# Optimization experiments

Measured on AMD Instinct MI355X. Metric: run time of the kernel, lower is better.

Reference implementation:

```python
import jax, jax.numpy as jnp
import numpy as np

N_NODES = 50000
E_EDGES = 1600000
D = 256


def setup_inputs() -> dict:
    key = jax.random.key(0)
    ks = jax.random.split(key, 10)
    inp = {
        "x": jax.random.normal(ks[0], (N_NODES, D), dtype=jnp.float32),
        "W0": jax.random.normal(ks[1], (D, D), dtype=jnp.float32) * (1.0 / np.sqrt(D)),
        "W1": jax.random.normal(ks[2], (D, D), dtype=jnp.float32) * (1.0 / np.sqrt(D)),
        "b": jnp.zeros((D,), dtype=jnp.float32),
        "src0": jax.random.randint(ks[3], (E_EDGES,), 0, N_NODES, dtype=jnp.int32),
        "dst0": jax.random.randint(ks[4], (E_EDGES,), 0, N_NODES, dtype=jnp.int32),
        "val0": jax.random.uniform(ks[5], (E_EDGES,), dtype=jnp.float32),
        "src1": jax.random.randint(ks[6], (E_EDGES,), 0, N_NODES, dtype=jnp.int32),
        "dst1": jax.random.randint(ks[7], (E_EDGES,), 0, N_NODES, dtype=jnp.int32),
        "val1": jax.random.uniform(ks[8], (E_EDGES,), dtype=jnp.float32),
    }
    return inp


def _spmm(src, dst, val, dense, num_segments):
    # sparse [N,N] (COO: A[dst, src] = val) @ dense [N,D] -> [N,D]
    # gather rows of dense at src, scale by edge value, scatter-add to dst
    return jax.ops.segment_sum(val[:, None] * dense[src], dst, num_segments=num_segments)


def reference(x, W0, W1, b, src0, dst0, val0, src1, dst1, val1):
    n = x.shape[0]
    # per-support dense GEMM then SpMM, summed over supports (2 supports)
    out = _spmm(src0, dst0, val0, x @ W0, n)
    out = out + _spmm(src1, dst1, val1, x @ W1, n)
    out = out + b  # bias
    return jax.nn.relu(out)  # act = F.relu
```

## Files before the change

### kernel.cpp

```cpp
#include <hip/hip_runtime.h>

#define D 256
#define CAP 64
#define CAP_S 60
#define OVFCAP 16384
#define BCAP 10240
#define CHUNK 8192

typedef __attribute__((ext_vector_type(8))) short short8;
typedef __attribute__((ext_vector_type(4))) float f32x4;

__device__ inline ushort f2bf(float f) {
  unsigned u = __float_as_uint(f);
  unsigned r = (u + 0x7FFF + ((u >> 16) & 1)) >> 16;
  return (ushort)r;
}
__device__ inline float bf_lo(unsigned u) { return __uint_as_float(u << 16); }
__device__ inline float bf_hi(unsigned u) { return __uint_as_float(u & 0xFFFF0000u); }

__global__ __launch_bounds__(256) void prep_kernel(const float* __restrict__ W0,
                                                   const float* __restrict__ W1,
                                                   ushort* __restrict__ Wt0,
                                                   ushort* __restrict__ Wt1,
                                                   int* __restrict__ gz, int ngz) {
  if (blockIdx.x < 128) {
    const int blk = blockIdx.x;
    const float* W = (blk >> 6) ? W1 : W0;
    ushort* Wt = (blk >> 6) ? Wt1 : Wt0;
    __shared__ float t[32][33];
    int tx = threadIdx.x & 31, ty = threadIdx.x >> 5;
    int k0 = (blk & 7) * 32, n0 = ((blk >> 3) & 7) * 32;
    for (int r = ty; r < 32; r += 8)
      t[r][tx] = W[(size_t)(k0 + r) * D + n0 + tx];
    __syncthreads();
    for (int r = ty; r < 32; r += 8)
      Wt[(size_t)(n0 + r) * D + k0 + tx] = f2bf(t[tx][r]);
  } else {
    int nb = gridDim.x - 128;
    for (int i = (blockIdx.x - 128) * 256 + threadIdx.x; i < ngz; i += nb * 256)
      gz[i] = 0;
  }
}

__device__ __forceinline__ void gemm_body(const float* __restrict__ A,
                                          const ushort* __restrict__ Bt,
                                          ushort* __restrict__ C, int M,
                                          int blk, int mtiles) {
  __shared__ ushort As[128 * 40];
  __shared__ ushort Bs[128 * 40];
  const int tid = threadIdx.x;
  const int bm = (blk % mtiles) * 128;
  const int bn = (blk / mtiles) * 128;
  const int wave = tid >> 6, lane = tid & 63;
  const int wm = wave & 1, wn = wave >> 1;
  const int lr = lane & 15;
  const int kg = lane >> 4;
  f32x4 acc[4][4];
#pragma unroll
  for (int m = 0; m < 4; ++m)
#pragma unroll
    for (int n = 0; n < 4; ++n) acc[m][n] = (f32x4){0.f, 0.f, 0.f, 0.f};

  for (int k0 = 0; k0 < D; k0 += 32) {
    __syncthreads();
#pragma unroll
    for (int c = 0; c < 4; ++c) {
      int linear = c * 256 + tid;
      int row = linear >> 3;
      int f4 = linear & 7;
      int gr = bm + row;
      float4 a = (gr < M) ? *(const float4*)(A + (size_t)gr * D + k0 + f4 * 4)
                          : make_float4(0.f, 0.f, 0.f, 0.f);
      ushort4 o;
      o.x = f2bf(a.x); o.y = f2bf(a.y); o.z = f2bf(a.z); o.w = f2bf(a.w);
      *(ushort4*)&As[row * 40 + f4 * 4] = o;
    }
#pragma unroll
    for (int c = 0; c < 2; ++c) {
      int linear = c * 256 + tid;
      int row = linear >> 2;
      int part = linear & 3;
      uint4 w4 = *(const uint4*)(Bt + (size_t)(bn + row) * D + k0 + part * 8);
      *(uint4*)&Bs[row * 40 + part * 8] = w4;
    }
    __syncthreads();
    short8 af[4], bfr[4];
#pragma unroll
    for (int m = 0; m < 4; ++m)
      af[m] = *(const short8*)&As[(wm * 64 + m * 16 + lr) * 40 + kg * 8];
#pragma unroll
    for (int n = 0; n < 4; ++n)
      bfr[n] = *(const short8*)&Bs[(wn * 64 + n * 16 + lr) * 40 + kg * 8];
#pragma unroll
    for (int m = 0; m < 4; ++m)
#pragma unroll
      for (int n = 0; n < 4; ++n)
        acc[m][n] = __builtin_amdgcn_mfma_f32_16x16x32_bf16(af[m], bfr[n], acc[m][n], 0, 0, 0);
  }

#pragma unroll
  for (int m = 0; m < 4; ++m)
#pragma unroll
    for (int j = 0; j < 4; ++j) {
      int gr = bm + wm * 64 + m * 16 + kg * 4 + j;
      if (gr < M) {
#pragma unroll
        for (int n = 0; n < 4; ++n) {
          int gc = bn + wn * 64 + n * 16 + lr;
          C[(size_t)gr * D + gc] = f2bf(acc[m][n][j]);
        }
      }
    }
}

__device__ __forceinline__ void binA_body(const int* __restrict__ src,
                                          const int* __restrict__ dst,
                                          const float* __restrict__ val, int E,
                                          int* __restrict__ gcur,
                                          int2* __restrict__ binned,
                                          int* __restrict__ ovfc, int4* __restrict__ ovf,
                                          int nbkt, int blk) {
  __shared__ int hist[200];
  __shared__ int base[200];
  const int tid = threadIdx.x;
  for (int i = tid; i < nbkt; i += 256) hist[i] = 0;
  __syncthreads();
  const int e0 = blk * CHUNK;
  const int e1 = min(E, e0 + CHUNK);
  for (int e = e0 + tid; e < e1; e += 256)
    atomicAdd(&hist[dst[e] >> 8], 1);
  __syncthreads();
  for (int i = tid; i < nbkt; i += 256) {
    int h = hist[i];
    base[i] = h ? atomicAdd(&gcur[i], h) : 0;
    hist[i] = 0;
  }
  __syncthreads();
  for (int e = e0 + tid; e < e1; e += 256) {
    int d = dst[e];
    int s = src[e];
    int vb = __float_as_int(val[e]);
    int k = d >> 8;
    int pos = base[k] + atomicAdd(&hist[k], 1);
    if (pos < BCAP) {
      binned[(size_t)k * BCAP + pos] = make_int2(((d & 255) << 16) | s, vb);
    } else {
      int o = atomicAdd(ovfc, 1);
      if (o < OVFCAP) ovf[o] = make_int4(d, s, vb, 0);
    }
  }
}

__global__ __launch_bounds__(256) void passB(const int2* __restrict__ binned,
                                             const int* __restrict__ gcur,
                                             uint* __restrict__ padded,
                                             int* __restrict__ cnt,
                                             int* __restrict__ ovfc, int4* __restrict__ ovf) {
  __shared__ int lcnt[256];
  __shared__ uint stage[256 * CAP_S];
  const int b = blockIdx.x;
  const int tid = threadIdx.x;
  lcnt[tid] = 0;
  __syncthreads();
  const int n = min(gcur[b], BCAP);
  const int2* bp = binned + (size_t)b * BCAP;
  for (int i = tid; i < n; i += 256) {
    int2 e = bp[i];
    int dlow = (e.x >> 16) & 255;
    int s = atomicAdd(&lcnt[dlow], 1);
    if (s < CAP_S) {
      float v = __int_as_float(e.y);
      stage[dlow * CAP_S + s] = (uint)(e.x & 0xFFFF) | ((uint)f2bf(v) << 16);
    } else {
      int o = atomicAdd(ovfc, 1);
      if (o < OVFCAP) ovf[o] = make_int4((b << 8) + dlow, e.x & 0xFFFF, e.y, 0);
    }
  }
  __syncthreads();
  const int row = (b << 8) + tid;
  const int written = min(lcnt[tid], CAP_S);
  cnt[row] = written;
  uint4* dp = (uint4*)(padded + ((size_t)row << 6));
  const uint4* sp = (const uint4*)&stage[tid * CAP_S];
  const int nq = (written + 3) >> 2;
  for (int q = 0; q < nq; ++q) dp[q] = sp[q];
}

template <int FINAL>
__device__ __forceinline__ void spmm_body(const ushort* __restrict__ H,
                                          const uint* __restrict__ padded,
                                          const int* __restrict__ cnt,
                                          float* __restrict__ out,
                                          const float* __restrict__ bias, int N,
                                          int blk) {
  const int row = blk * 4 + (threadIdx.x >> 6);
  if (row >= N) return;
  const int lane = threadIdx.x & 63;
  const int c = min(cnt[row], CAP);
  const uint4* ep4 = (const uint4*)(padded + ((size_t)row << 6));
  float4 acc = make_float4(0.f, 0.f, 0.f, 0.f);
  const int nchunk = (c + 3) >> 2;
  if (nchunk > 0) {
    uint4 cur = ep4[0];
    for (int j = 0; j < nchunk; ++j) {
      uint4 nxt = (j + 1 < nchunk) ? ep4[j + 1] : cur;
      int b4 = j << 2;
#pragma unroll
      for (int k = 0; k < 4; ++k) {
        uint e = (k == 0) ? cur.x : (k == 1) ? cur.y : (k == 2) ? cur.z : cur.w;
        bool ok = (b4 + k) < c;
        uint sidx = ok ? (e & 0xFFFFu) : 0u;
        float v = ok ? __uint_as_float(e & 0xFFFF0000u) : 0.f;
        uint2 h = *((const uint2*)(H + (size_t)sidx * D) + lane);
        acc.x += v * bf_lo(h.x);
        acc.y += v * bf_hi(h.x);
        acc.z += v * bf_lo(h.y);
        acc.w += v * bf_hi(h.y);
      }
      cur = nxt;
    }
  }
  float4* op = (float4*)(out + (size_t)row * D) + lane;
  if (FINAL) {
    float4 o = *op;
    float4 bb = ((const float4*)bias)[lane];
    o.x = fmaxf(o.x + acc.x + bb.x, 0.f);
    o.y = fmaxf(o.y + acc.y + bb.y, 0.f);
    o.z = fmaxf(o.z + acc.z + bb.z, 0.f);
    o.w = fmaxf(o.w + acc.w + bb.w, 0.f);
    *op = o;
  } else {
    *op = acc;
  }
}

__global__ __launch_bounds__(256) void fatA(
    const float* __restrict__ A, const ushort* __restrict__ Bt0, ushort* __restrict__ H,
    int M, int mtiles,
    const int* __restrict__ src0, const int* __restrict__ dst0, const float* __restrict__ val0,
    int E0, int* __restrict__ gcur0, int2* __restrict__ binned0, int* __restrict__ ovfc0,
    int4* __restrict__ ovf0,
    const int* __restrict__ src1, const int* __restrict__ dst1, const float* __restrict__ val1,
    int E1, int* __restrict__ gcur1, int2* __restrict__ binned1, int* __restrict__ ovfc1,
    int4* __restrict__ ovf1,
    int nbkt, int nbA0, int nbA1) {
  const int bid = blockIdx.x;
  if (bid < nbA0)
    binA_body(src0, dst0, val0, E0, gcur0, binned0, ovfc0, ovf0, nbkt, bid);
  else if (bid < nbA0 + nbA1)
    binA_body(src1, dst1, val1, E1, gcur1, binned1, ovfc1, ovf1, nbkt, bid - nbA0);
  else
    gemm_body(A, Bt0, H, M, bid - nbA0 - nbA1, mtiles);
}

__global__ __launch_bounds__(256) void gemm_plain(const float* __restrict__ A,
                                                  const ushort* __restrict__ Bt,
                                                  ushort* __restrict__ C, int M, int mtiles) {
  gemm_body(A, Bt, C, M, blockIdx.x, mtiles);
}

__global__ __launch_bounds__(256) void spmm_first(const ushort* __restrict__ H,
                                                  const uint* __restrict__ padded,
                                                  const int* __restrict__ cnt,
                                                  float* __restrict__ out,
                                                  const float* __restrict__ bias, int N) {
  spmm_body<0>(H, padded, cnt, out, bias, N, blockIdx.x);
}

__global__ __launch_bounds__(256) void spmm_final(const ushort* __restrict__ H,
                                                  const uint* __restrict__ padded,
                                                  const int* __restrict__ cnt,
                                                  float* __restrict__ out,
                                                  const float* __restrict__ bias, int N) {
  spmm_body<1>(H, padded, cnt, out, bias, N, blockIdx.x);
}

__global__ void overflow_add(const int* __restrict__ ovfc, const int4* __restrict__ ovf,
                             const ushort* __restrict__ H, float* __restrict__ out) {
  int n = min(*ovfc, OVFCAP);
  int w = (blockIdx.x * blockDim.x + threadIdx.x) >> 6;
  int lane = threadIdx.x & 63;
  int nw = (gridDim.x * blockDim.x) >> 6;
  for (int i = w; i < n; i += nw) {
    int4 r = ovf[i];
    uint2 h = *((const uint2*)(H + (size_t)r.y * D) + lane);
    float v = __int_as_float(r.z);
    float* op = out + (size_t)r.x * D + (lane << 2);
    unsafeAtomicAdd(op + 0, v * bf_lo(h.x));
    unsafeAtomicAdd(op + 1, v * bf_hi(h.x));
    unsafeAtomicAdd(op + 2, v * bf_lo(h.y));
    unsafeAtomicAdd(op + 3, v * bf_hi(h.y));
  }
}

extern "C" void kernel_launch(void* const* d_in, const int* in_sizes, int n_in,
                              void* d_out, int out_size, void* d_ws, size_t ws_size,
                              hipStream_t stream) {
  const float* x    = (const float*)d_in[0];
  const float* W0   = (const float*)d_in[1];
  const float* W1   = (const float*)d_in[2];
  const float* b    = (const float*)d_in[3];
  const int*   src0 = (const int*)d_in[4];
  const int*   dst0 = (const int*)d_in[5];
  const float* val0 = (const float*)d_in[6];
  const int*   src1 = (const int*)d_in[7];
  const int*   dst1 = (const int*)d_in[8];
  const float* val1 = (const float*)d_in[9];
  float* out = (float*)d_out;

  const int N  = in_sizes[0] / D;
  const int E0 = in_sizes[4];
  const int E1 = in_sizes[7];
  const int nbkt = (N + 255) >> 8;
  const int nrows = nbkt << 8;

  char* w = (char*)d_ws;
  auto align = [](size_t v) { return (v + 255) & ~(size_t)255; };
  ushort* H       = (ushort*)w; w += align((size_t)N * D * 2);
  ushort* Wt0     = (ushort*)w; w += align((size_t)D * D * 2);
  ushort* Wt1     = (ushort*)w; w += align((size_t)D * D * 2);
  int2*   binned0 = (int2*)w;   w += align((size_t)nbkt * BCAP * 8);
  int2*   binned1 = (int2*)w;   w += align((size_t)nbkt * BCAP * 8);
  uint*   padded0 = (uint*)w;   w += align((size_t)nrows * CAP * 4);
  uint*   padded1 = (uint*)binned0;
  int*    cnt0    = (int*)w;    w += align((size_t)nrows * 4);
  int*    cnt1    = (int*)w;    w += align((size_t)nrows * 4);
  int*    gz      = (int*)w;    w += align((size_t)(2 * nbkt + 2) * 4);
  int4*   ovf0    = (int4*)w;   w += align((size_t)OVFCAP * 16);
  int4*   ovf1    = (int4*)w;   w += align((size_t)OVFCAP * 16);
  int* gcur0 = gz;
  int* gcur1 = gz + nbkt;
  int* ovfc0 = gz + 2 * nbkt;
  int* ovfc1 = gz + 2 * nbkt + 1;

  const int mtiles = (N + 127) / 128;
  const int NGB = mtiles * 2;
  const int nbA0 = (E0 + CHUNK - 1) / CHUNK;
  const int nbA1 = (E1 + CHUNK - 1) / CHUNK;
  const int NPB = (N + 3) / 4;

  prep_kernel<<<130, 256, 0, stream>>>(W0, W1, Wt0, Wt1, gz, 2 * nbkt + 2);
  fatA<<<nbA0 + nbA1 + NGB, 256, 0, stream>>>(
      x, Wt0, H, N, mtiles,
      src0, dst0, val0, E0, gcur0, binned0, ovfc0, ovf0,
      src1, dst1, val1, E1, gcur1, binned1, ovfc1, ovf1,
      nbkt, nbA0, nbA1);
  passB<<<nbkt, 256, 0, stream>>>(binned0, gcur0, padded0, cnt0, ovfc0, ovf0);
  spmm_first<<<NPB, 256, 0, stream>>>(H, padded0, cnt0, out, b, N);
  overflow_add<<<16, 256, 0, stream>>>(ovfc0, ovf0, H, out);
  gemm_plain<<<NGB, 256, 0, stream>>>(x, Wt1, H, N, mtiles);
  passB<<<nbkt, 256, 0, stream>>>(binned1, gcur1, padded1, cnt1, ovfc1, ovf1);
  overflow_add<<<16, 256, 0, stream>>>(ovfc1, ovf1, H, out);
  spmm_final<<<NPB, 256, 0, stream>>>(H, padded1, cnt1, out, b, N);
}
```

Measured before the change: 344.1 us.

## Fuse both supports' GEMMs, binning passes and SpMMs into single launches

When the workspace is large enough, both support GEMMs now run in one combined launch with separate H buffers, both passB binnings run in one grid, and a single fused SpMM kernel gathers both supports per row and applies bias and ReLU. Overflow rows are zeroed and flagged beforehand so the fused kernel can add the atomically accumulated overflow contributions. The gather loop is also rewritten to double-buffer index and H-row loads, so gathers are issued ahead of the multiply-adds. This drops the intermediate write and re-read of the output and gives each launch more parallelism, at the cost of extra workspace and a fallback path if the workspace is too small.

```diff
diff --git a/kernel.cpp b/kernel.cpp
--- a/kernel.cpp
+++ b/kernel.cpp
@@ -151,14 +151,14 @@
   }
 }
 
-__global__ __launch_bounds__(256) void passB(const int2* __restrict__ binned,
-                                             const int* __restrict__ gcur,
-                                             uint* __restrict__ padded,
-                                             int* __restrict__ cnt,
-                                             int* __restrict__ ovfc, int4* __restrict__ ovf) {
+__device__ __forceinline__ void passB_body(const int2* __restrict__ binned,
+                                           const int* __restrict__ gcur,
+                                           uint* __restrict__ padded,
+                                           int* __restrict__ cnt,
+                                           int* __restrict__ ovfc, int4* __restrict__ ovf,
+                                           int b) {
   __shared__ int lcnt[256];
   __shared__ uint stage[256 * CAP_S];
-  const int b = blockIdx.x;
   const int tid = threadIdx.x;
   lcnt[tid] = 0;
   __syncthreads();
@@ -180,10 +180,75 @@
   const int row = (b << 8) + tid;
   const int written = min(lcnt[tid], CAP_S);
   cnt[row] = written;
+  const int nq = (written + 3) >> 2;
+  for (int s = written; s < (nq << 2); ++s) stage[tid * CAP_S + s] = 0;
   uint4* dp = (uint4*)(padded + ((size_t)row << 6));
   const uint4* sp = (const uint4*)&stage[tid * CAP_S];
-  const int nq = (written + 3) >> 2;
   for (int q = 0; q < nq; ++q) dp[q] = sp[q];
+}
+
+__global__ __launch_bounds__(256) void passB(const int2* __restrict__ binned,
+                                             const int* __restrict__ gcur,
+                                             uint* __restrict__ padded,
+                                             int* __restrict__ cnt,
+                                             int* __restrict__ ovfc, int4* __restrict__ ovf) {
+  passB_body(binned, gcur, padded, cnt, ovfc, ovf, blockIdx.x);
+}
+
+__global__ __launch_bounds__(256) void passBoth(
+    const int2* __restrict__ binned0, const int* __restrict__ gcur0, uint* __restrict__ padded0,
+    int* __restrict__ cnt0, int* __restrict__ ovfc0, int4* __restrict__ ovf0,
+    const int2* __restrict__ binned1, const int* __restrict__ gcur1, uint* __restrict__ padded1,
+    int* __restrict__ cnt1, int* __restrict__ ovfc1, int4* __restrict__ ovf1, int nbkt) {
+  if (blockIdx.x < nbkt)
+    passB_body(binned0, gcur0, padded0, cnt0, ovfc0, ovf0, blockIdx.x);
+  else
+    passB_body(binned1, gcur1, padded1, cnt1, ovfc1, ovf1, blockIdx.x - nbkt);
+}
+
+__device__ __forceinline__ void gather_acc(const ushort* __restrict__ H,
+                                           const uint* __restrict__ padded,
+                                           int row, int c, int lane, float4& acc) {
+  const int nc = (c + 3) >> 2;
+  if (nc <= 0) return;
+  const uint4* ep4 = (const uint4*)(padded + ((size_t)row << 6));
+  const uint2* Hl = (const uint2*)H + lane;
+
+  uint2 h0[4], h1[4];
+  float v0[4], v1[4];
+
+#define GA_ISSUE(S, J)                                                  \
+  do {                                                                  \
+    uint4 m = ep4[(J)];                                                 \
+    uint ee[4] = {m.x, m.y, m.z, m.w};                                  \
+    _Pragma("unroll") for (int k = 0; k < 4; ++k) {                     \
+      v##S[k] = __uint_as_float(ee[k] & 0xFFFF0000u);                   \
+      h##S[k] = Hl[(size_t)(ee[k] & 0xFFFFu) << 6];                     \
+    }                                                                   \
+  } while (0)
+
+#define GA_COMP(S)                                                      \
+  do {                                                                  \
+    _Pragma("unroll") for (int k = 0; k < 4; ++k) {                     \
+      acc.x += v##S[k] * bf_lo(h##S[k].x);                              \
+      acc.y += v##S[k] * bf_hi(h##S[k].x);                              \
+      acc.z += v##S[k] * bf_lo(h##S[k].y);                              \
+      acc.w += v##S[k] * bf_hi(h##S[k].y);                              \
+    }                                                                   \
+  } while (0)
+
+  GA_ISSUE(0, 0);
+  if (nc > 1) GA_ISSUE(1, 1);
+  int j = 0;
+  for (; j + 1 < nc; j += 2) {
+    GA_COMP(0);
+    if (j + 2 < nc) GA_ISSUE(0, j + 2);
+    GA_COMP(1);
+    if (j + 3 < nc) GA_ISSUE(1, j + 3);
+  }
+  if (j < nc) GA_COMP(0);
+#undef GA_ISSUE
+#undef GA_COMP
 }
 
 template <int FINAL>
@@ -196,30 +261,8 @@
   const int row = blk * 4 + (threadIdx.x >> 6);
   if (row >= N) return;
   const int lane = threadIdx.x & 63;
-  const int c = min(cnt[row], CAP);
-  const uint4* ep4 = (const uint4*)(padded + ((size_t)row << 6));
   float4 acc = make_float4(0.f, 0.f, 0.f, 0.f);
-  const int nchunk = (c + 3) >> 2;
-  if (nchunk > 0) {
-    uint4 cur = ep4[0];
-    for (int j = 0; j < nchunk; ++j) {
-      uint4 nxt = (j + 1 < nchunk) ? ep4[j + 1] : cur;
-      int b4 = j << 2;
-#pragma unroll
-      for (int k = 0; k < 4; ++k) {
-        uint e = (k == 0) ? cur.x : (k == 1) ? cur.y : (k == 2) ? cur.z : cur.w;
-        bool ok = (b4 + k) < c;
-        uint sidx = ok ? (e & 0xFFFFu) : 0u;
-        float v = ok ? __uint_as_float(e & 0xFFFF0000u) : 0.f;
-        uint2 h = *((const uint2*)(H + (size_t)sidx * D) + lane);
-        acc.x += v * bf_lo(h.x);
-        acc.y += v * bf_hi(h.x);
-        acc.z += v * bf_lo(h.y);
-        acc.w += v * bf_hi(h.y);
-      }
-      cur = nxt;
-    }
-  }
+  gather_acc(H, padded, row, min(cnt[row], CAP), lane, acc);
   float4* op = (float4*)(out + (size_t)row * D) + lane;
   if (FINAL) {
     float4 o = *op;
@@ -232,6 +275,45 @@
   } else {
     *op = acc;
   }
+}
+
+__global__ __launch_bounds__(256) void spmm_first(const ushort* __restrict__ H,
+                                                  const uint* __restrict__ padded,
+                                                  const int* __restrict__ cnt,
+                                                  float* __restrict__ out,
+                                                  const float* __restrict__ bias, int N) {
+  spmm_body<0>(H, padded, cnt, out, bias, N, blockIdx.x);
+}
+
+__global__ __launch_bounds__(256) void spmm_final(const ushort* __restrict__ H,
+                                                  const uint* __restrict__ padded,
+                                                  const int* __restrict__ cnt,
+                                                  float* __restrict__ out,
+                                                  const float* __restrict__ bias, int N) {
+  spmm_body<1>(H, padded, cnt, out, bias, N, blockIdx.x);
+}
+
+__global__ __launch_bounds__(256) void spmm_fused(
+    const ushort* __restrict__ H0, const uint* __restrict__ padded0, const int* __restrict__ cnt0,
+    const ushort* __restrict__ H1, const uint* __restrict__ padded1, const int* __restrict__ cnt1,
+    float* __restrict__ out, const float* __restrict__ bias,
+    const int* __restrict__ rowflag, int N) {
+  const int row = blockIdx.x * 4 + (threadIdx.x >> 6);
+  if (row >= N) return;
+  const int lane = threadIdx.x & 63;
+  float4 acc = make_float4(0.f, 0.f, 0.f, 0.f);
+  gather_acc(H0, padded0, row, min(cnt0[row], CAP), lane, acc);
+  gather_acc(H1, padded1, row, min(cnt1[row], CAP), lane, acc);
+  float4* op = (float4*)(out + (size_t)row * D) + lane;
+  float4 bb = ((const float4*)bias)[lane];
+  float4 base = make_float4(0.f, 0.f, 0.f, 0.f);
+  if (rowflag[row]) base = *op;
+  float4 o;
+  o.x = fmaxf(acc.x + bb.x + base.x, 0.f);
+  o.y = fmaxf(acc.y + bb.y + base.y, 0.f);
+  o.z = fmaxf(acc.z + bb.z + base.z, 0.f);
+  o.w = fmaxf(acc.w + bb.w + base.w, 0.f);
+  *op = o;
 }
 
 __global__ __launch_bounds__(256) void fatA(
@@ -253,26 +335,46 @@
     gemm_body(A, Bt0, H, M, bid - nbA0 - nbA1, mtiles);
 }
 
+__global__ __launch_bounds__(256) void fatA2(
+    const float* __restrict__ A, const ushort* __restrict__ Bt0, const ushort* __restrict__ Bt1,
+    ushort* __restrict__ H0, ushort* __restrict__ H1, int M, int mtiles,
+    const int* __restrict__ src0, const int* __restrict__ dst0, const float* __restrict__ val0,
+    int E0, int* __restrict__ gcur0, int2* __restrict__ binned0, int* __restrict__ ovfc0,
+    int4* __restrict__ ovf0,
+    const int* __restrict__ src1, const int* __restrict__ dst1, const float* __restrict__ val1,
+    int E1, int* __restrict__ gcur1, int2* __restrict__ binned1, int* __restrict__ ovfc1,
+    int4* __restrict__ ovf1,
+    int nbkt, int nbA0, int nbA1, int NGB) {
+  const int bid = blockIdx.x;
+  if (bid < nbA0)
+    binA_body(src0, dst0, val0, E0, gcur0, binned0, ovfc0, ovf0, nbkt, bid);
+  else if (bid < nbA0 + nbA1)
+    binA_body(src1, dst1, val1, E1, gcur1, binned1, ovfc1, ovf1, nbkt, bid - nbA0);
+  else if (bid < nbA0 + nbA1 + NGB)
+    gemm_body(A, Bt0, H0, M, bid - nbA0 - nbA1, mtiles);
+  else
+    gemm_body(A, Bt1, H1, M, bid - nbA0 - nbA1 - NGB, mtiles);
+}
+
 __global__ __launch_bounds__(256) void gemm_plain(const float* __restrict__ A,
                                                   const ushort* __restrict__ Bt,
                                                   ushort* __restrict__ C, int M, int mtiles) {
   gemm_body(A, Bt, C, M, blockIdx.x, mtiles);
 }
 
-__global__ __launch_bounds__(256) void spmm_first(const ushort* __restrict__ H,
-                                                  const uint* __restrict__ padded,
-                                                  const int* __restrict__ cnt,
-                                                  float* __restrict__ out,
-                                                  const float* __restrict__ bias, int N) {
-  spmm_body<0>(H, padded, cnt, out, bias, N, blockIdx.x);
-}
-
-__global__ __launch_bounds__(256) void spmm_final(const ushort* __restrict__ H,
-                                                  const uint* __restrict__ padded,
-                                                  const int* __restrict__ cnt,
-                                                  float* __restrict__ out,
-                                                  const float* __restrict__ bias, int N) {
-  spmm_body<1>(H, padded, cnt, out, bias, N, blockIdx.x);
+__global__ void ovf_zero(const int* __restrict__ ovfc0, const int4* __restrict__ ovf0,
+                         const int* __restrict__ ovfc1, const int4* __restrict__ ovf1,
+                         float* __restrict__ out, int* __restrict__ rowflag) {
+  int n0 = min(*ovfc0, OVFCAP);
+  int n1 = min(*ovfc1, OVFCAP);
+  int w = (blockIdx.x * blockDim.x + threadIdx.x) >> 6;
+  int lane = threadIdx.x & 63;
+  int nw = (gridDim.x * blockDim.x) >> 6;
+  for (int i = w; i < n0 + n1; i += nw) {
+    int d = (i < n0) ? ovf0[i].x : ovf1[i - n0].x;
+    if (lane == 0) rowflag[d] = 1;
+    ((float4*)(out + (size_t)d * D))[lane] = make_float4(0.f, 0.f, 0.f, 0.f);
+  }
 }
 
 __global__ void overflow_add(const int* __restrict__ ovfc, const int4* __restrict__ ovf,
@@ -314,42 +416,84 @@
   const int nbkt = (N + 255) >> 8;
   const int nrows = nbkt << 8;
 
-  char* w = (char*)d_ws;
-  auto align = [](size_t v) { return (v + 255) & ~(size_t)255; };
-  ushort* H       = (ushort*)w; w += align((size_t)N * D * 2);
-  ushort* Wt0     = (ushort*)w; w += align((size_t)D * D * 2);
-  ushort* Wt1     = (ushort*)w; w += align((size_t)D * D * 2);
-  int2*   binned0 = (int2*)w;   w += align((size_t)nbkt * BCAP * 8);
-  int2*   binned1 = (int2*)w;   w += align((size_t)nbkt * BCAP * 8);
-  uint*   padded0 = (uint*)w;   w += align((size_t)nrows * CAP * 4);
-  uint*   padded1 = (uint*)binned0;
-  int*    cnt0    = (int*)w;    w += align((size_t)nrows * 4);
-  int*    cnt1    = (int*)w;    w += align((size_t)nrows * 4);
-  int*    gz      = (int*)w;    w += align((size_t)(2 * nbkt + 2) * 4);
-  int4*   ovf0    = (int4*)w;   w += align((size_t)OVFCAP * 16);
-  int4*   ovf1    = (int4*)w;   w += align((size_t)OVFCAP * 16);
-  int* gcur0 = gz;
-  int* gcur1 = gz + nbkt;
-  int* ovfc0 = gz + 2 * nbkt;
-  int* ovfc1 = gz + 2 * nbkt + 1;
-
   const int mtiles = (N + 127) / 128;
   const int NGB = mtiles * 2;
   const int nbA0 = (E0 + CHUNK - 1) / CHUNK;
   const int nbA1 = (E1 + CHUNK - 1) / CHUNK;
   const int NPB = (N + 3) / 4;
 
-  prep_kernel<<<130, 256, 0, stream>>>(W0, W1, Wt0, Wt1, gz, 2 * nbkt + 2);
-  fatA<<<nbA0 + nbA1 + NGB, 256, 0, stream>>>(
-      x, Wt0, H, N, mtiles,
-      src0, dst0, val0, E0, gcur0, binned0, ovfc0, ovf0,
-      src1, dst1, val1, E1, gcur1, binned1, ovfc1, ovf1,
-      nbkt, nbA0, nbA1);
-  passB<<<nbkt, 256, 0, stream>>>(binned0, gcur0, padded0, cnt0, ovfc0, ovf0);
-  spmm_first<<<NPB, 256, 0, stream>>>(H, padded0, cnt0, out, b, N);
-  overflow_add<<<16, 256, 0, stream>>>(ovfc0, ovf0, H, out);
-  gemm_plain<<<NGB, 256, 0, stream>>>(x, Wt1, H, N, mtiles);
-  passB<<<nbkt, 256, 0, stream>>>(binned1, gcur1, padded1, cnt1, ovfc1, ovf1);
-  overflow_add<<<16, 256, 0, stream>>>(ovfc1, ovf1, H, out);
-  spmm_final<<<NPB, 256, 0, stream>>>(H, padded1, cnt1, out, b, N);
-}
+  size_t off = 0;
+  auto alloc = [&](size_t bytes) -> void* {
+    void* p = (char*)d_ws + off;
+    off = (off + bytes + 255) & ~(size_t)255;
+    return p;
+  };
+
+  ushort* H0      = (ushort*)alloc((size_t)N * D * 2);
+  ushort* H1      = (ushort*)alloc((size_t)N * D * 2);
+  ushort* Wt0     = (ushort*)alloc((size_t)D * D * 2);
+  ushort* Wt1     = (ushort*)alloc((size_t)D * D * 2);
+  int2*   binned0 = (int2*)alloc((size_t)nbkt * BCAP * 8);
+  int2*   binned1 = (int2*)alloc((size_t)nbkt * BCAP * 8);
+  uint*   padded0 = (uint*)alloc((size_t)nrows * CAP * 4);
+  uint*   padded1 = (uint*)alloc((size_t)nrows * CAP * 4);
+  int*    cnt0    = (int*)alloc((size_t)nrows * 4);
+  int*    cnt1    = (int*)alloc((size_t)nrows * 4);
+  int*    gzall   = (int*)alloc((size_t)(2 * nbkt + 2 + nrows) * 4);
+  int4*   ovf0    = (int4*)alloc((size_t)OVFCAP * 16);
+  int4*   ovf1    = (int4*)alloc((size_t)OVFCAP * 16);
+  const bool fused = (off <= ws_size);
+
+  if (!fused) {
+    off = 0;
+    H0      = (ushort*)alloc((size_t)N * D * 2);
+    H1      = H0;
+    Wt0     = (ushort*)alloc((size_t)D * D * 2);
+    Wt1     = (ushort*)alloc((size_t)D * D * 2);
+    binned0 = (int2*)alloc((size_t)nbkt * BCAP * 8);
+    binned1 = (int2*)alloc((size_t)nbkt * BCAP * 8);
+    padded0 = (uint*)alloc((size_t)nrows * CAP * 4);
+    padded1 = (uint*)binned0;
+    cnt0    = (int*)alloc((size_t)nrows * 4);
+    cnt1    = (int*)alloc((size_t)nrows * 4);
+    gzall   = (int*)alloc((size_t)(2 * nbkt + 2) * 4);
+    ovf0    = (int4*)alloc((size_t)OVFCAP * 16);
+    ovf1    = (int4*)alloc((size_t)OVFCAP * 16);
+  }
+
+  int* gcur0   = gzall;
+  int* gcur1   = gzall + nbkt;
+  int* ovfc0   = gzall + 2 * nbkt;
+  int* ovfc1   = gzall + 2 * nbkt + 1;
+  int* rowflag = gzall + 2 * nbkt + 2;
+
+  if (fused) {
+    prep_kernel<<<160, 256, 0, stream>>>(W0, W1, Wt0, Wt1, gzall, 2 * nbkt + 2 + nrows);
+    fatA2<<<nbA0 + nbA1 + 2 * NGB, 256, 0, stream>>>(
+        x, Wt0, Wt1, H0, H1, N, mtiles,
+        src0, dst0, val0, E0, gcur0, binned0, ovfc0, ovf0,
+        src1, dst1, val1, E1, gcur1, binned1, ovfc1, ovf1,
+        nbkt, nbA0, nbA1, NGB);
+    passBoth<<<2 * nbkt, 256, 0, stream>>>(binned0, gcur0, padded0, cnt0, ovfc0, ovf0,
+                                           binned1, gcur1, padded1, cnt1, ovfc1, ovf1, nbkt);
+    ovf_zero<<<16, 256, 0, stream>>>(ovfc0, ovf0, ovfc1, ovf1, out, rowflag);
+    overflow_add<<<16, 256, 0, stream>>>(ovfc0, ovf0, H0, out);
+    overflow_add<<<16, 256, 0, stream>>>(ovfc1, ovf1, H1, out);
+    spmm_fused<<<NPB, 256, 0, stream>>>(H0, padded0, cnt0, H1, padded1, cnt1,
+                                        out, b, rowflag, N);
+  } else {
+    prep_kernel<<<160, 256, 0, stream>>>(W0, W1, Wt0, Wt1, gzall, 2 * nbkt + 2);
+    fatA<<<nbA0 + nbA1 + NGB, 256, 0, stream>>>(
+        x, Wt0, H0, N, mtiles,
+        src0, dst0, val0, E0, gcur0, binned0, ovfc0, ovf0,
+        src1, dst1, val1, E1, gcur1, binned1, ovfc1, ovf1,
+        nbkt, nbA0, nbA1);
+    passB<<<nbkt, 256, 0, stream>>>(binned0, gcur0, padded0, cnt0, ovfc0, ovf0);
+    spmm_first<<<NPB, 256, 0, stream>>>(H0, padded0, cnt0, out, b, N);
+    overflow_add<<<16, 256, 0, stream>>>(ovfc0, ovf0, H0, out);
+    gemm_plain<<<NGB, 256, 0, stream>>>(x, Wt1, H0, N, mtiles);
+    passB<<<nbkt, 256, 0, stream>>>(binned1, gcur1, padded1, cnt1, ovfc1, ovf1);
+    overflow_add<<<16, 256, 0, stream>>>(ovfc1, ovf1, H0, out);
+    spmm_final<<<NPB, 256, 0, stream>>>(H0, padded1, cnt1, out, b, N);
+  }
+}
```

Result: faster. 322.1 us (-6.4%).
